# Performance work log

Hardware: AMD Instinct MI355X
Metric: run time of the kernel (lower is better)

Reference implementation:

```python
import jax, jax.numpy as jnp
import numpy as np

N = 8192
D = 1024
THRESHOLD = 0.85
LN_EPS = 1e-5
NORM_EPS = 1e-12


def setup_inputs() -> dict:
    key = jax.random.key(0)
    ks = jax.random.split(key, 3)
    scale = 0.02
    return {
        "summaries": jax.random.normal(ks[0], (N, D), dtype=jnp.float32),
        "W1": jax.random.normal(ks[1], (D, D), dtype=jnp.float32) * scale,
        "b1": jnp.zeros((D,), dtype=jnp.float32),
        "gamma": jnp.ones((D,), dtype=jnp.float32),
        "beta": jnp.zeros((D,), dtype=jnp.float32),
        "W2": jax.random.normal(ks[2], (D, D), dtype=jnp.float32) * scale,
        "b2": jnp.zeros((D,), dtype=jnp.float32),
    }


def reference(summaries, W1, b1, gamma, beta, W2, b2):
    # dedup_encoder: Linear -> LayerNorm -> GELU(exact) -> Linear
    h = summaries @ W1 + b1                      # [N, D]
    mu = jnp.mean(h, axis=-1, keepdims=True)
    var = jnp.var(h, axis=-1, keepdims=True)
    h = (h - mu) * jax.lax.rsqrt(var + LN_EPS) * gamma + beta
    h = jax.nn.gelu(h, approximate=False)
    enc = h @ W2 + b2                            # [N, D]
    # F.normalize(p=2, dim=-1)
    norm = jnp.linalg.norm(enc, axis=-1, keepdims=True)
    enc = enc / jnp.maximum(norm, NORM_EPS)
    # cosine similarity matrix
    sim = enc @ enc.T                            # [N, N]
    # suppression: j is duplicate if any i<j has sim[i,j] > threshold
    # (equivalent to the original triu_indices loop: duplicates also suppress)
    hot = jnp.triu(sim > THRESHOLD, k=1)         # [N, N] bool, strict upper
    is_duplicate = jnp.any(hot, axis=0)          # [N] bool
    return sim, is_duplicate
```

## Files before the change

### kernel.cpp

```cpp
#include <hip/hip_runtime.h>
#include <hip/hip_bf16.h>

#define NROWS 8192
#define DIM   1024
#define THRESH 0.85f

typedef __attribute__((ext_vector_type(4))) float f32x4;
typedef __attribute__((ext_vector_type(8))) short bf16x8;

__device__ __forceinline__ short f2bf(float x) {
    union { float f; unsigned u; } c; c.f = x;
    unsigned r = c.u + 0x7FFFu + ((c.u >> 16) & 1u);
    return (short)(r >> 16);
}

__device__ __forceinline__ void async16(const void* g, void* l) {
    __builtin_amdgcn_global_load_lds(
        (const __attribute__((address_space(1))) void*)g,
        (__attribute__((address_space(3))) void*)l, 16, 0, 0);
}


__global__ __launch_bounds__(256) void f32_to_bf16_k(const float* __restrict__ in,
                                                     short* __restrict__ out, int n) {
    int i = (blockIdx.x * 256 + threadIdx.x) * 4;
    if (i < n) {
        float4 v = *(const float4*)(in + i);
        short4 o;
        o.x = f2bf(v.x); o.y = f2bf(v.y); o.z = f2bf(v.z); o.w = f2bf(v.w);
        *(short4*)(out + i) = o;
    }
}

__global__ __launch_bounds__(256) void transpose_to_bf16_k(const float* __restrict__ in,
                                                           short* __restrict__ out, int dim) {
    __shared__ float tile[32][33];
    int bx = blockIdx.x * 32, by = blockIdx.y * 32;
    int tx = threadIdx.x, ty = threadIdx.y;
    for (int r = ty; r < 32; r += 8) tile[r][tx] = in[(size_t)(by + r) * dim + bx + tx];
    __syncthreads();
    for (int r = ty; r < 32; r += 8) out[(size_t)(bx + r) * dim + by + tx] = f2bf(tile[tx][r]);
}

__global__ void zero_f32_k(float* p, int n) {
    int i = blockIdx.x * blockDim.x + threadIdx.x;
    if (i < n) p[i] = 0.f;
}

__global__ __launch_bounds__(256) void ln_gelu_k(const float* __restrict__ h,
                                                 const float* __restrict__ gamma,
                                                 const float* __restrict__ beta,
                                                 short* __restrict__ g) {
    int row = blockIdx.x, t = threadIdx.x;
    const float* x = h + (size_t)row * DIM;
    float lv[4], s = 0.f, ss = 0.f;
    #pragma unroll
    for (int i = 0; i < 4; i++) {
        float v = x[t + i * 256];
        lv[i] = v; s += v; ss += v * v;
    }
    #pragma unroll
    for (int o = 32; o; o >>= 1) { s += __shfl_down(s, o, 64); ss += __shfl_down(ss, o, 64); }
    __shared__ float red[8];
    if ((t & 63) == 0) { red[(t >> 6) * 2] = s; red[(t >> 6) * 2 + 1] = ss; }
    __syncthreads();
    s  = red[0] + red[2] + red[4] + red[6];
    ss = red[1] + red[3] + red[5] + red[7];
    float mu = s * (1.0f / DIM);
    float var = ss * (1.0f / DIM) - mu * mu;
    float rstd = rsqrtf(var + 1e-5f);
    short* go = g + (size_t)row * DIM;
    #pragma unroll
    for (int i = 0; i < 4; i++) {
        int c = t + i * 256;
        float v = (lv[i] - mu) * rstd * gamma[c] + beta[c];
        float ge = 0.5f * v * (1.0f + erff(v * 0.70710678118654752f));
        go[c] = f2bf(ge);
    }
}

__global__ __launch_bounds__(256) void rownorm_bf16_k(const float* __restrict__ enc,
                                                      short* __restrict__ out) {
    int row = blockIdx.x, t = threadIdx.x;
    const float* x = enc + (size_t)row * DIM;
    float lv[4], ss = 0.f;
    #pragma unroll
    for (int i = 0; i < 4; i++) {
        float v = x[t + i * 256];
        lv[i] = v; ss += v * v;
    }
    #pragma unroll
    for (int o = 32; o; o >>= 1) ss += __shfl_down(ss, o, 64);
    __shared__ float red[4];
    if ((t & 63) == 0) red[t >> 6] = ss;
    __syncthreads();
    ss = red[0] + red[1] + red[2] + red[3];
    float inv = 1.0f / fmaxf(sqrtf(ss), 1e-12f);
    short* go = out + (size_t)row * DIM;
    #pragma unroll
    for (int i = 0; i < 4; i++) go[t + i * 256] = f2bf(lv[i] * inv);
}

__global__ __launch_bounds__(256) void gemm_bt_k(const short* __restrict__ A,
                                                 const short* __restrict__ Bt,
                                                 float* __restrict__ C,
                                                 const float* __restrict__ bias,
                                                 float* __restrict__ dup,
                                                 int M, int Nmat, int K, int mode) {
    __shared__ __align__(16) char smraw[17024];
    short* smA = (short*)smraw;
    short* smB = smA + 128 * 32;
    float* epi = (float*)smraw;

    int bm, bn;
    if (mode == 1) {
        const int NB = Nmat >> 7;
        int bid = blockIdx.x, r = 0, off = 0;
        while (off + (NB - r) <= bid) { off += NB - r; r++; }
        bm = r; bn = r + (bid - off);
    } else {
        bn = blockIdx.x; bm = blockIdx.y;
    }
    const int tileN = bn * 128;
    const int tileM = bm * 128;

    const int t = threadIdx.x;
    const int wave = t >> 6;
    const int wm = wave >> 1, wn = wave & 1;
    const int l = t & 63;

    const int sr = t >> 2;
    const int swr = (sr & 3) ^ ((sr >> 2) & 3);
    const int cg = (((t & 3) ^ swr) & 3) * 8;
    const size_t aOff = (size_t)(tileM + sr) * K + cg;
    const size_t bOff = (size_t)(tileN + sr) * K + cg;
    const int ldsOff = t * 8;

    f32x4 acc[4][4];
    #pragma unroll
    for (int i = 0; i < 4; i++)
        #pragma unroll
        for (int j = 0; j < 4; j++) acc[i][j] = (f32x4){0.f, 0.f, 0.f, 0.f};

    const int lr = l & 15;
    const int lq = l >> 4;
    const int sw = (lr & 3) ^ ((lr >> 2) & 3);
    const int kg = (lq ^ sw) & 3;
    const int aBase = (wm * 64 + lr) * 32 + kg * 8;
    const int bBase = (wn * 64 + lr) * 32 + kg * 8;

    for (int k0 = 0; k0 < K; k0 += 32) {
        __syncthreads();
        async16(A + aOff + k0,                   smA + ldsOff);
        async16(A + aOff + (size_t)64 * K + k0,  smA + ldsOff + 64 * 32);
        async16(Bt + bOff + k0,                  smB + ldsOff);
        async16(Bt + bOff + (size_t)64 * K + k0, smB + ldsOff + 64 * 32);
        __syncthreads();

        bf16x8 af[4], bfr[4];
        #pragma unroll
        for (int i = 0; i < 4; i++) af[i] = *(const bf16x8*)(smA + aBase + i * 16 * 32);
        #pragma unroll
        for (int j = 0; j < 4; j++) bfr[j] = *(const bf16x8*)(smB + bBase + j * 16 * 32);
        #pragma unroll
        for (int i = 0; i < 4; i++)
            #pragma unroll
            for (int j = 0; j < 4; j++)
                acc[i][j] = __builtin_amdgcn_mfma_f32_16x16x32_bf16(af[i], bfr[j], acc[i][j], 0, 0, 0);
    }

    for (int ch = 0; ch < 4; ch++) {
        __syncthreads();
        #pragma unroll
        for (int j = 0; j < 4; j++) {
            const int cl = wn * 64 + j * 16 + lr;
            const float bj = bias ? bias[tileN + cl] : 0.f;
            #pragma unroll
            for (int r = 0; r < 4; r++) {
                const int rl = wm * 16 + lq * 4 + r;
                epi[rl * 132 + cl] = acc[ch][j][r] + bj;
            }
        }
        __syncthreads();
        #pragma unroll
        for (int k = 0; k < 4; k++) {
            const int v = k * 256 + t;
            const int rl = v >> 5;
            const int c4 = (v & 31) * 4;
            float4 vec = *(float4*)&epi[rl * 132 + c4];
            const int grow = tileM + (rl < 16 ? ch * 16 + rl : 48 + ch * 16 + rl);
            const int gcol = tileN + c4;
            *(float4*)&C[(size_t)grow * Nmat + gcol] = vec;
            if (mode == 1) {
                if (vec.x > THRESH && grow < gcol)     dup[gcol]     = 1.f;
                if (vec.y > THRESH && grow < gcol + 1) dup[gcol + 1] = 1.f;
                if (vec.z > THRESH && grow < gcol + 2) dup[gcol + 2] = 1.f;
                if (vec.w > THRESH && grow < gcol + 3) dup[gcol + 3] = 1.f;
            }
        }
    }

    if (mode == 1 && bm != bn) {
        const int mr = wn * 16 + lr;
        for (int ch = 0; ch < 4; ch++) {
            __syncthreads();
            #pragma unroll
            for (int i = 0; i < 4; i++) {
                #pragma unroll
                for (int r = 0; r < 4; r++) {
                    const int mc = wm * 64 + i * 16 + lq * 4 + r;
                    epi[mr * 132 + mc] = acc[i][ch][r];
                }
            }
            __syncthreads();
            #pragma unroll
            for (int k = 0; k < 4; k++) {
                const int v = k * 256 + t;
                const int rl = v >> 5;
                const int c4 = (v & 31) * 4;
                float4 vec = *(float4*)&epi[rl * 132 + c4];
                const int orow = tileN + ch * 16 + (rl < 16 ? rl : 48 + rl);
                *(float4*)&C[(size_t)orow * Nmat + tileM + c4] = vec;
            }
        }
    }
}


#define BARF()   do { asm volatile("" ::: "memory"); __builtin_amdgcn_s_barrier(); asm volatile("" ::: "memory"); } while (0)
#define LGKM0()  asm volatile("s_waitcnt lgkmcnt(0)" ::: "memory")
#define VMCNT(n) asm volatile("s_waitcnt vmcnt(" #n ")" ::: "memory")

__global__ __launch_bounds__(512, 2) void gemm256_tri_k(const short* __restrict__ E,
                                                        float* __restrict__ C,
                                                        float* __restrict__ dup,
                                                        int Nrows, int K) {
    extern __shared__ __align__(16) char smraw[];
    short* smA = (short*)smraw;
    short* smB = smA + 32768;
    float* epi = (float*)smraw;

    const int NBT = Nrows >> 8;
    int bid = blockIdx.x;
    int r = 0, off = 0;
    while (off + (NBT - r) <= bid) { off += NBT - r; r++; }
    const int bm = r, bn = r + (bid - off);
    const int tileM = bm << 8, tileN = bn << 8;

    const int t = threadIdx.x;
    const int wave = t >> 6;
    const int wm = wave >> 2, wn = wave & 3;
    const int l = t & 63;
    const int lr = l & 15, lq = l >> 4;

    const int srow  = t >> 2;
    const int sslot = ((t & 3) ^ ((t >> 2) & 3)) * 8;
    const short* aS0 = E + (size_t)(tileM + srow) * K + sslot;
    const short* aS1 = aS0 + (size_t)128 * K;
    const short* bS0 = E + (size_t)(tileN + srow) * K + sslot;
    const short* bS1 = bS0 + (size_t)128 * K;
    const int ldst = t * 8;

    const int swz  = (lq ^ (lr & 3)) * 8;
    const int aoff = (wm * 128 + lr) * 32 + swz;
    const int boff = (wn * 64  + lr) * 32 + swz;

    f32x4 acc[8][4];
    #pragma unroll
    for (int i = 0; i < 8; i++)
        #pragma unroll
        for (int j = 0; j < 4; j++) acc[i][j] = (f32x4){0.f, 0.f, 0.f, 0.f};

#define STAGE_A(DB, KH, KC) do { \
    short* d_ = smA + (DB) * 16384 + (KH) * 8192 + ldst; \
    async16(aS0 + (KC), d_); async16(aS1 + (KC), d_ + 4096); } while (0)
#define STAGE_B(DB, KH, KC) do { \
    short* d_ = smB + (DB) * 16384 + (KH) * 8192 + ldst; \
    async16(bS0 + (KC), d_); async16(bS1 + (KC), d_ + 4096); } while (0)

#define PH_AB(DB, KS, MB) do { \
    const short* Ab_ = smA + (DB) * 16384 + (KS) * 8192 + aoff; \
    const short* Bb_ = smB + (DB) * 16384 + (KS) * 8192 + boff; \
    af[0] = *(const bf16x8*)(Ab_ + ((MB) + 0) * 512); \
    af[1] = *(const bf16x8*)(Ab_ + ((MB) + 1) * 512); \
    af[2] = *(const bf16x8*)(Ab_ + ((MB) + 2) * 512); \
    af[3] = *(const bf16x8*)(Ab_ + ((MB) + 3) * 512); \
    bfr[0] = *(const bf16x8*)(Bb_ + 0);    \
    bfr[1] = *(const bf16x8*)(Bb_ + 512);  \
    bfr[2] = *(const bf16x8*)(Bb_ + 1024); \
    bfr[3] = *(const bf16x8*)(Bb_ + 1536); } while (0)

#define PH_A(DB, KS, MB) do { \
    const short* Ab_ = smA + (DB) * 16384 + (KS) * 8192 + aoff; \
    af[0] = *(const bf16x8*)(Ab_ + ((MB) + 0) * 512); \
    af[1] = *(const bf16x8*)(Ab_ + ((MB) + 1) * 512); \
    af[2] = *(const bf16x8*)(Ab_ + ((MB) + 2) * 512); \
    af[3] = *(const bf16x8*)(Ab_ + ((MB) + 3) * 512); } while (0)

#define MFMA16(MB) do { \
    __builtin_amdgcn_s_setprio(1); \
    _Pragma("unroll") for (int m_ = 0; m_ < 4; m_++) \
        _Pragma("unroll") for (int n_ = 0; n_ < 4; n_++) \
            acc[(MB) + m_][n_] = __builtin_amdgcn_mfma_f32_16x16x32_bf16(af[m_], bfr[n_], acc[(MB) + m_][n_], 0, 0, 0); \
    __builtin_amdgcn_s_setprio(0); } while (0)

    bf16x8 af[4], bfr[4];

    STAGE_A(0, 0, 0);  STAGE_B(0, 0, 0);
    STAGE_A(0, 1, 32); STAGE_B(0, 1, 32);
    STAGE_A(1, 0, 64); STAGE_B(1, 0, 64);
    VMCNT(4);
    BARF();

    const int NIT = K >> 7;
    for (int it = 0; it < NIT - 1; ++it) {
        const int kb = it * 128;
        PH_AB(0, 0, 0); STAGE_A(1, 1, kb + 96);  BARF(); LGKM0(); MFMA16(0); BARF();
        PH_A (0, 0, 4); STAGE_B(1, 1, kb + 96);  BARF(); LGKM0(); MFMA16(4); BARF();
        PH_AB(0, 1, 0); STAGE_A(0, 0, kb + 128); BARF(); LGKM0(); MFMA16(0); BARF();
        PH_A (0, 1, 4); STAGE_B(0, 0, kb + 128); BARF(); LGKM0(); MFMA16(4); VMCNT(4); BARF();
        PH_AB(1, 0, 0); STAGE_A(0, 1, kb + 160); BARF(); LGKM0(); MFMA16(0); BARF();
        PH_A (1, 0, 4); STAGE_B(0, 1, kb + 160); BARF(); LGKM0(); MFMA16(4); BARF();
        PH_AB(1, 1, 0); STAGE_A(1, 0, kb + 192); BARF(); LGKM0(); MFMA16(0); BARF();
        PH_A (1, 1, 4); STAGE_B(1, 0, kb + 192); BARF(); LGKM0(); MFMA16(4); VMCNT(4); BARF();
    }
    {
        const int kb = (NIT - 1) * 128;
        PH_AB(0, 0, 0); STAGE_A(1, 1, kb + 96);  BARF(); LGKM0(); MFMA16(0); BARF();
        PH_A (0, 0, 4); STAGE_B(1, 1, kb + 96);  BARF(); LGKM0(); MFMA16(4); BARF();
        PH_AB(0, 1, 0);                          BARF(); LGKM0(); MFMA16(0); BARF();
        PH_A (0, 1, 4);                          BARF(); LGKM0(); MFMA16(4); VMCNT(0); BARF();
        PH_AB(1, 0, 0);                          BARF(); LGKM0(); MFMA16(0); BARF();
        PH_A (1, 0, 4);                          BARF(); LGKM0(); MFMA16(4); BARF();
        PH_AB(1, 1, 0);                          BARF(); LGKM0(); MFMA16(0); BARF();
        PH_A (1, 1, 4);                          BARF(); LGKM0(); MFMA16(4); BARF();
    }

#undef STAGE_A
#undef STAGE_B
#undef PH_AB
#undef PH_A
#undef MFMA16

    __syncthreads();
    for (int rr = 0; rr < 4; rr++) {
        if ((rr >> 1) == wm) {
            const int mb = (rr & 1) * 4;
            #pragma unroll
            for (int m = 0; m < 4; m++)
                #pragma unroll
                for (int n = 0; n < 4; n++)
                    #pragma unroll
                    for (int q = 0; q < 4; q++)
                        epi[(m * 16 + lq * 4 + q) * 260 + wn * 64 + n * 16 + lr] = acc[mb + m][n][q];
        }
        __syncthreads();
        #pragma unroll
        for (int k2 = 0; k2 < 8; k2++) {
            const int v = k2 * 512 + t;
            const int rl = v >> 6;
            const int c4 = (v & 63) * 4;
            float4 vec = *(float4*)&epi[rl * 260 + c4];
            const int grow = tileM + rr * 64 + rl;
            const int gcol = tileN + c4;
            *(float4*)&C[(size_t)grow * Nrows + gcol] = vec;
            if (vec.x > THRESH && grow < gcol)     dup[gcol]     = 1.f;
            if (vec.y > THRESH && grow < gcol + 1) dup[gcol + 1] = 1.f;
            if (vec.z > THRESH && grow < gcol + 2) dup[gcol + 2] = 1.f;
            if (vec.w > THRESH && grow < gcol + 3) dup[gcol + 3] = 1.f;
        }
        __syncthreads();
    }

    if (bm != bn) {
        for (int cc = 0; cc < 4; cc++) {
            if (wn == cc) {
                #pragma unroll
                for (int i2 = 0; i2 < 8; i2++)
                    #pragma unroll
                    for (int n = 0; n < 4; n++)
                        #pragma unroll
                        for (int q = 0; q < 4; q++)
                            epi[(n * 16 + lr) * 260 + wm * 128 + i2 * 16 + lq * 4 + q] = acc[i2][n][q];
            }
            __syncthreads();
            #pragma unroll
            for (int k2 = 0; k2 < 8; k2++) {
                const int v = k2 * 512 + t;
                const int rl = v >> 6;
                const int c4 = (v & 63) * 4;
                float4 vec = *(float4*)&epi[rl * 260 + c4];
                *(float4*)&C[(size_t)(tileN + cc * 64 + rl) * Nrows + tileM + c4] = vec;
            }
            __syncthreads();
        }
    }
}


extern "C" void kernel_launch(void* const* d_in, const int* in_sizes, int n_in,
                              void* d_out, int out_size, void* d_ws, size_t ws_size,
                              hipStream_t stream) {
    const float* summaries = (const float*)d_in[0];
    const float* W1    = (const float*)d_in[1];
    const float* b1    = (const float*)d_in[2];
    const float* gamma = (const float*)d_in[3];
    const float* beta  = (const float*)d_in[4];
    const float* W2    = (const float*)d_in[5];
    const float* b2    = (const float*)d_in[6];

    float* sim = (float*)d_out;
    float* dup = sim + (size_t)NROWS * NROWS;

    char* ws = (char*)d_ws;
    float* hbuf = (float*)ws;
    short* xb   = (short*)(ws + (size_t)32 * 1024 * 1024);
    short* gbuf = (short*)(ws + (size_t)48 * 1024 * 1024);
    short* w1t  = (short*)(ws + (size_t)64 * 1024 * 1024);
    short* w2t  = (short*)(ws + (size_t)66 * 1024 * 1024);

    static int tri_init = 0;
    if (!tri_init) {
        hipFuncSetAttribute(reinterpret_cast<const void*>(gemm256_tri_k),
                            hipFuncAttributeMaxDynamicSharedMemorySize, 131072);
        tri_init = 1;
    }

    f32_to_bf16_k<<<dim3(NROWS * DIM / 1024), dim3(256), 0, stream>>>(summaries, xb, NROWS * DIM);
    transpose_to_bf16_k<<<dim3(32, 32), dim3(32, 8), 0, stream>>>(W1, w1t, DIM);
    transpose_to_bf16_k<<<dim3(32, 32), dim3(32, 8), 0, stream>>>(W2, w2t, DIM);
    zero_f32_k<<<dim3(32), dim3(256), 0, stream>>>(dup, NROWS);

    gemm_bt_k<<<dim3(DIM / 128, NROWS / 128), dim3(256), 0, stream>>>(
        xb, w1t, hbuf, b1, (float*)nullptr, NROWS, DIM, DIM, 0);
    ln_gelu_k<<<dim3(NROWS), dim3(256), 0, stream>>>(hbuf, gamma, beta, gbuf);
    gemm_bt_k<<<dim3(DIM / 128, NROWS / 128), dim3(256), 0, stream>>>(
        gbuf, w2t, hbuf, b2, (float*)nullptr, NROWS, DIM, DIM, 0);
    rownorm_bf16_k<<<dim3(NROWS), dim3(256), 0, stream>>>(hbuf, xb);
    const int NBT = NROWS / 256;
    gemm256_tri_k<<<dim3(NBT * (NBT + 1) / 2), dim3(512), 131072, stream>>>(
        xb, sim, dup, NROWS, DIM);
}
```

Baseline: 495.4 us.

## Replace encoder GEMMs with pipelined 128x256 kernel, vectorize LN/norm, remap tri blocks

Swaps the simple single-buffered 128x128 GEMM used for both encoder linears for a 512-thread 128x256 kernel. The new kernel double-buffers its async global-to-LDS loads with explicit waitcnt and barrier scheduling and raises MFMA priority, to hide load latency behind compute. The LayerNorm+GELU and row-normalize kernels now use float4 loads and short4 stores. The triangular similarity kernel gets a block-id remap that interleaves work across groups of eight, changing the order tiles are scheduled across compute units. This adds LDS pressure (96KB) and hand-tuned waitcnt counts that must match the issued loads.

```diff
diff --git a/kernel.cpp b/kernel.cpp
--- a/kernel.cpp
+++ b/kernel.cpp
@@ -53,12 +53,9 @@
                                                  short* __restrict__ g) {
     int row = blockIdx.x, t = threadIdx.x;
     const float* x = h + (size_t)row * DIM;
-    float lv[4], s = 0.f, ss = 0.f;
-    #pragma unroll
-    for (int i = 0; i < 4; i++) {
-        float v = x[t + i * 256];
-        lv[i] = v; s += v; ss += v * v;
-    }
+    float4 v4 = *(const float4*)(x + t * 4);
+    float s = v4.x + v4.y + v4.z + v4.w;
+    float ss = v4.x * v4.x + v4.y * v4.y + v4.z * v4.z + v4.w * v4.w;
     #pragma unroll
     for (int o = 32; o; o >>= 1) { s += __shfl_down(s, o, 64); ss += __shfl_down(ss, o, 64); }
     __shared__ float red[8];
@@ -69,26 +66,28 @@
     float mu = s * (1.0f / DIM);
     float var = ss * (1.0f / DIM) - mu * mu;
     float rstd = rsqrtf(var + 1e-5f);
-    short* go = g + (size_t)row * DIM;
+    float4 g4 = *(const float4*)(gamma + t * 4);
+    float4 b4 = *(const float4*)(beta + t * 4);
+    float vv[4] = {v4.x, v4.y, v4.z, v4.w};
+    float gg[4] = {g4.x, g4.y, g4.z, g4.w};
+    float bb[4] = {b4.x, b4.y, b4.z, b4.w};
+    short4 o;
+    short* op = (short*)&o;
     #pragma unroll
     for (int i = 0; i < 4; i++) {
-        int c = t + i * 256;
-        float v = (lv[i] - mu) * rstd * gamma[c] + beta[c];
+        float v = (vv[i] - mu) * rstd * gg[i] + bb[i];
         float ge = 0.5f * v * (1.0f + erff(v * 0.70710678118654752f));
-        go[c] = f2bf(ge);
-    }
+        op[i] = f2bf(ge);
+    }
+    *(short4*)(g + (size_t)row * DIM + t * 4) = o;
 }
 
 __global__ __launch_bounds__(256) void rownorm_bf16_k(const float* __restrict__ enc,
                                                       short* __restrict__ out) {
     int row = blockIdx.x, t = threadIdx.x;
     const float* x = enc + (size_t)row * DIM;
-    float lv[4], ss = 0.f;
-    #pragma unroll
-    for (int i = 0; i < 4; i++) {
-        float v = x[t + i * 256];
-        lv[i] = v; ss += v * v;
-    }
+    float4 v4 = *(const float4*)(x + t * 4);
+    float ss = v4.x * v4.x + v4.y * v4.y + v4.z * v4.z + v4.w * v4.w;
     #pragma unroll
     for (int o = 32; o; o >>= 1) ss += __shfl_down(ss, o, 64);
     __shared__ float red[4];
@@ -96,45 +95,45 @@
     __syncthreads();
     ss = red[0] + red[1] + red[2] + red[3];
     float inv = 1.0f / fmaxf(sqrtf(ss), 1e-12f);
-    short* go = out + (size_t)row * DIM;
-    #pragma unroll
-    for (int i = 0; i < 4; i++) go[t + i * 256] = f2bf(lv[i] * inv);
-}
-
-__global__ __launch_bounds__(256) void gemm_bt_k(const short* __restrict__ A,
-                                                 const short* __restrict__ Bt,
-                                                 float* __restrict__ C,
-                                                 const float* __restrict__ bias,
-                                                 float* __restrict__ dup,
-                                                 int M, int Nmat, int K, int mode) {
-    __shared__ __align__(16) char smraw[17024];
+    short4 o;
+    o.x = f2bf(v4.x * inv); o.y = f2bf(v4.y * inv);
+    o.z = f2bf(v4.z * inv); o.w = f2bf(v4.w * inv);
+    *(short4*)(out + (size_t)row * DIM + t * 4) = o;
+}
+
+#define BARF()   do { asm volatile("" ::: "memory"); __builtin_amdgcn_s_barrier(); asm volatile("" ::: "memory"); } while (0)
+#define LGKM0()  asm volatile("s_waitcnt lgkmcnt(0)" ::: "memory")
+#define VMCNT(n) asm volatile("s_waitcnt vmcnt(" #n ")" ::: "memory")
+
+__global__ __launch_bounds__(512, 2) void gemm_dense256_k(const short* __restrict__ A,
+                                                          const short* __restrict__ Bt,
+                                                          float* __restrict__ C,
+                                                          const float* __restrict__ bias,
+                                                          int M, int Nmat, int K) {
+    extern __shared__ __align__(16) char smraw[];
     short* smA = (short*)smraw;
-    short* smB = smA + 128 * 32;
+    short* smB = smA + 16384;
     float* epi = (float*)smraw;
 
-    int bm, bn;
-    if (mode == 1) {
-        const int NB = Nmat >> 7;
-        int bid = blockIdx.x, r = 0, off = 0;
-        while (off + (NB - r) <= bid) { off += NB - r; r++; }
-        bm = r; bn = r + (bid - off);
-    } else {
-        bn = blockIdx.x; bm = blockIdx.y;
-    }
-    const int tileN = bn * 128;
-    const int tileM = bm * 128;
+    const int tileN = blockIdx.x << 8;
+    const int tileM = blockIdx.y << 7;
 
     const int t = threadIdx.x;
     const int wave = t >> 6;
-    const int wm = wave >> 1, wn = wave & 1;
+    const int wm = wave >> 2, wn = wave & 3;
     const int l = t & 63;
-
-    const int sr = t >> 2;
-    const int swr = (sr & 3) ^ ((sr >> 2) & 3);
-    const int cg = (((t & 3) ^ swr) & 3) * 8;
-    const size_t aOff = (size_t)(tileM + sr) * K + cg;
-    const size_t bOff = (size_t)(tileN + sr) * K + cg;
-    const int ldsOff = t * 8;
+    const int lr = l & 15, lq = l >> 4;
+
+    const int srow  = t >> 2;
+    const int sslot = ((t & 3) ^ ((t >> 2) & 3)) * 8;
+    const short* aS  = A  + (size_t)(tileM + srow) * K + sslot;
+    const short* bS0 = Bt + (size_t)(tileN + srow) * K + sslot;
+    const short* bS1 = bS0 + (size_t)128 * K;
+    const int t8 = t * 8;
+
+    const int swz  = (lq ^ (lr & 3)) * 8;
+    const int aoff = (wm * 64 + lr) * 32 + swz;
+    const int boff = (wn * 64 + lr) * 32 + swz;
 
     f32x4 acc[4][4];
     #pragma unroll
@@ -142,94 +141,84 @@
         #pragma unroll
         for (int j = 0; j < 4; j++) acc[i][j] = (f32x4){0.f, 0.f, 0.f, 0.f};
 
-    const int lr = l & 15;
-    const int lq = l >> 4;
-    const int sw = (lr & 3) ^ ((lr >> 2) & 3);
-    const int kg = (lq ^ sw) & 3;
-    const int aBase = (wm * 64 + lr) * 32 + kg * 8;
-    const int bBase = (wn * 64 + lr) * 32 + kg * 8;
-
-    for (int k0 = 0; k0 < K; k0 += 32) {
-        __syncthreads();
-        async16(A + aOff + k0,                   smA + ldsOff);
-        async16(A + aOff + (size_t)64 * K + k0,  smA + ldsOff + 64 * 32);
-        async16(Bt + bOff + k0,                  smB + ldsOff);
-        async16(Bt + bOff + (size_t)64 * K + k0, smB + ldsOff + 64 * 32);
-        __syncthreads();
-
-        bf16x8 af[4], bfr[4];
-        #pragma unroll
-        for (int i = 0; i < 4; i++) af[i] = *(const bf16x8*)(smA + aBase + i * 16 * 32);
-        #pragma unroll
-        for (int j = 0; j < 4; j++) bfr[j] = *(const bf16x8*)(smB + bBase + j * 16 * 32);
-        #pragma unroll
-        for (int i = 0; i < 4; i++)
+#define DSTAGE(DB, KH, KC) do { \
+    short* da_ = smA + (DB) * 8192 + (KH) * 4096 + t8; \
+    async16(aS + (KC), da_); \
+    short* db_ = smB + (DB) * 16384 + (KH) * 8192 + t8; \
+    async16(bS0 + (KC), db_); async16(bS1 + (KC), db_ + 4096); } while (0)
+
+#define DPH(DB, KH) do { \
+    const short* Ab_ = smA + (DB) * 8192 + (KH) * 4096 + aoff; \
+    const short* Bb_ = smB + (DB) * 16384 + (KH) * 8192 + boff; \
+    af[0] = *(const bf16x8*)(Ab_ + 0);    af[1] = *(const bf16x8*)(Ab_ + 512); \
+    af[2] = *(const bf16x8*)(Ab_ + 1024); af[3] = *(const bf16x8*)(Ab_ + 1536); \
+    bfr[0] = *(const bf16x8*)(Bb_ + 0);    bfr[1] = *(const bf16x8*)(Bb_ + 512); \
+    bfr[2] = *(const bf16x8*)(Bb_ + 1024); bfr[3] = *(const bf16x8*)(Bb_ + 1536); } while (0)
+
+#define DMFMA16() do { \
+    __builtin_amdgcn_s_setprio(1); \
+    _Pragma("unroll") for (int m_ = 0; m_ < 4; m_++) \
+        _Pragma("unroll") for (int n_ = 0; n_ < 4; n_++) \
+            acc[m_][n_] = __builtin_amdgcn_mfma_f32_16x16x32_bf16(af[m_], bfr[n_], acc[m_][n_], 0, 0, 0); \
+    __builtin_amdgcn_s_setprio(0); } while (0)
+
+    bf16x8 af[4], bfr[4];
+
+    DSTAGE(0, 0, 0);
+    DSTAGE(0, 1, 32);
+    DSTAGE(1, 0, 64);
+    VMCNT(6);
+    BARF();
+
+    const int NIT = K >> 7;
+    for (int it = 0; it < NIT - 1; ++it) {
+        const int kb = it * 128;
+        DPH(0, 0); DSTAGE(1, 1, kb + 96);  BARF(); LGKM0(); DMFMA16(); VMCNT(6); BARF();
+        DPH(0, 1); DSTAGE(0, 0, kb + 128); BARF(); LGKM0(); DMFMA16(); VMCNT(6); BARF();
+        DPH(1, 0); DSTAGE(0, 1, kb + 160); BARF(); LGKM0(); DMFMA16(); VMCNT(6); BARF();
+        DPH(1, 1); DSTAGE(1, 0, kb + 192); BARF(); LGKM0(); DMFMA16(); VMCNT(6); BARF();
+    }
+    {
+        const int kb = (NIT - 1) * 128;
+        DPH(0, 0); DSTAGE(1, 1, kb + 96);  BARF(); LGKM0(); DMFMA16(); VMCNT(6); BARF();
+        DPH(0, 1);                         BARF(); LGKM0(); DMFMA16(); VMCNT(3); BARF();
+        DPH(1, 0);                         BARF(); LGKM0(); DMFMA16(); VMCNT(0); BARF();
+        DPH(1, 1);                         BARF(); LGKM0(); DMFMA16();           BARF();
+    }
+
+#undef DSTAGE
+#undef DPH
+#undef DMFMA16
+
+    float bj[4];
+    #pragma unroll
+    for (int nb = 0; nb < 4; nb++) bj[nb] = bias[tileN + wn * 64 + nb * 16 + lr];
+    __syncthreads();
+    for (int rr = 0; rr < 4; rr++) {
+        if (wm == (rr >> 1)) {
             #pragma unroll
-            for (int j = 0; j < 4; j++)
-                acc[i][j] = __builtin_amdgcn_mfma_f32_16x16x32_bf16(af[i], bfr[j], acc[i][j], 0, 0, 0);
-    }
-
-    for (int ch = 0; ch < 4; ch++) {
-        __syncthreads();
-        #pragma unroll
-        for (int j = 0; j < 4; j++) {
-            const int cl = wn * 64 + j * 16 + lr;
-            const float bj = bias ? bias[tileN + cl] : 0.f;
-            #pragma unroll
-            for (int r = 0; r < 4; r++) {
-                const int rl = wm * 16 + lq * 4 + r;
-                epi[rl * 132 + cl] = acc[ch][j][r] + bj;
+            for (int h = 0; h < 2; h++) {
+                const int mb = (rr & 1) * 2 + h;
+                #pragma unroll
+                for (int nb = 0; nb < 4; nb++)
+                    #pragma unroll
+                    for (int q = 0; q < 4; q++)
+                        epi[(h * 16 + lq * 4 + q) * 260 + wn * 64 + nb * 16 + lr] = acc[mb][nb][q] + bj[nb];
             }
         }
         __syncthreads();
         #pragma unroll
-        for (int k = 0; k < 4; k++) {
-            const int v = k * 256 + t;
-            const int rl = v >> 5;
-            const int c4 = (v & 31) * 4;
-            float4 vec = *(float4*)&epi[rl * 132 + c4];
-            const int grow = tileM + (rl < 16 ? ch * 16 + rl : 48 + ch * 16 + rl);
-            const int gcol = tileN + c4;
-            *(float4*)&C[(size_t)grow * Nmat + gcol] = vec;
-            if (mode == 1) {
-                if (vec.x > THRESH && grow < gcol)     dup[gcol]     = 1.f;
-                if (vec.y > THRESH && grow < gcol + 1) dup[gcol + 1] = 1.f;
-                if (vec.z > THRESH && grow < gcol + 2) dup[gcol + 2] = 1.f;
-                if (vec.w > THRESH && grow < gcol + 3) dup[gcol + 3] = 1.f;
-            }
+        for (int k2 = 0; k2 < 4; k2++) {
+            const int v = k2 * 512 + t;
+            const int rl = v >> 6;
+            const int c4 = (v & 63) * 4;
+            float4 vec = *(float4*)&epi[rl * 260 + c4];
+            *(float4*)&C[(size_t)(tileM + rr * 32 + rl) * Nmat + tileN + c4] = vec;
         }
-    }
-
-    if (mode == 1 && bm != bn) {
-        const int mr = wn * 16 + lr;
-        for (int ch = 0; ch < 4; ch++) {
-            __syncthreads();
-            #pragma unroll
-            for (int i = 0; i < 4; i++) {
-                #pragma unroll
-                for (int r = 0; r < 4; r++) {
-                    const int mc = wm * 64 + i * 16 + lq * 4 + r;
-                    epi[mr * 132 + mc] = acc[i][ch][r];
-                }
-            }
-            __syncthreads();
-            #pragma unroll
-            for (int k = 0; k < 4; k++) {
-                const int v = k * 256 + t;
-                const int rl = v >> 5;
-                const int c4 = (v & 31) * 4;
-                float4 vec = *(float4*)&epi[rl * 132 + c4];
-                const int orow = tileN + ch * 16 + (rl < 16 ? rl : 48 + rl);
-                *(float4*)&C[(size_t)orow * Nmat + tileM + c4] = vec;
-            }
-        }
-    }
-}
-
-
-#define BARF()   do { asm volatile("" ::: "memory"); __builtin_amdgcn_s_barrier(); asm volatile("" ::: "memory"); } while (0)
-#define LGKM0()  asm volatile("s_waitcnt lgkmcnt(0)" ::: "memory")
-#define VMCNT(n) asm volatile("s_waitcnt vmcnt(" #n ")" ::: "memory")
+        __syncthreads();
+    }
+}
+
 
 __global__ __launch_bounds__(512, 2) void gemm256_tri_k(const short* __restrict__ E,
                                                         float* __restrict__ C,
@@ -241,7 +230,12 @@
     float* epi = (float*)smraw;
 
     const int NBT = Nrows >> 8;
+    const int nwg = (NBT * (NBT + 1)) >> 1;
     int bid = blockIdx.x;
+    if (!(nwg & 7)) {
+        const int chunk = nwg >> 3;
+        bid = (bid & 7) * chunk + (bid >> 3);
+    }
     int r = 0, off = 0;
     while (off + (NBT - r) <= bid) { off += NBT - r; r++; }
     const int bm = r, bn = r + (bid - off);
@@ -419,11 +413,13 @@
     short* w1t  = (short*)(ws + (size_t)64 * 1024 * 1024);
     short* w2t  = (short*)(ws + (size_t)66 * 1024 * 1024);
 
-    static int tri_init = 0;
-    if (!tri_init) {
+    static int lds_init = 0;
+    if (!lds_init) {
         hipFuncSetAttribute(reinterpret_cast<const void*>(gemm256_tri_k),
                             hipFuncAttributeMaxDynamicSharedMemorySize, 131072);
-        tri_init = 1;
+        hipFuncSetAttribute(reinterpret_cast<const void*>(gemm_dense256_k),
+                            hipFuncAttributeMaxDynamicSharedMemorySize, 98304);
+        lds_init = 1;
     }
 
     f32_to_bf16_k<<<dim3(NROWS * DIM / 1024), dim3(256), 0, stream>>>(summaries, xb, NROWS * DIM);
@@ -431,11 +427,11 @@
     transpose_to_bf16_k<<<dim3(32, 32), dim3(32, 8), 0, stream>>>(W2, w2t, DIM);
     zero_f32_k<<<dim3(32), dim3(256), 0, stream>>>(dup, NROWS);
 
-    gemm_bt_k<<<dim3(DIM / 128, NROWS / 128), dim3(256), 0, stream>>>(
-        xb, w1t, hbuf, b1, (float*)nullptr, NROWS, DIM, DIM, 0);
+    gemm_dense256_k<<<dim3(DIM / 256, NROWS / 128), dim3(512), 98304, stream>>>(
+        xb, w1t, hbuf, b1, NROWS, DIM, DIM);
     ln_gelu_k<<<dim3(NROWS), dim3(256), 0, stream>>>(hbuf, gamma, beta, gbuf);
-    gemm_bt_k<<<dim3(DIM / 128, NROWS / 128), dim3(256), 0, stream>>>(
-        gbuf, w2t, hbuf, b2, (float*)nullptr, NROWS, DIM, DIM, 0);
+    gemm_dense256_k<<<dim3(DIM / 256, NROWS / 128), dim3(512), 98304, stream>>>(
+        gbuf, w2t, hbuf, b2, NROWS, DIM, DIM);
     rownorm_bf16_k<<<dim3(NROWS), dim3(256), 0, stream>>>(hbuf, xb);
     const int NBT = NROWS / 256;
     gemm256_tri_k<<<dim3(NBT * (NBT + 1) / 2), dim3(512), 131072, stream>>>(
```

After: 480.9 us. 2.9% less time.
